# Optimization experiments

Measured on AMD Instinct MI355X. Metric: run time of the kernel, lower is better.

The kernel has to match this reference:

```python
import jax, jax.numpy as jnp
import numpy as np

B, S, D, H = 4, 1024, 1024, 16
HD = D // H
NEG = 10000.0


def setup_inputs() -> dict:
    key = jax.random.key(0)
    k1, k2, k3 = jax.random.split(key, 3)
    std = 0.02
    return {
        "x": jax.random.normal(k1, (B, S, D), dtype=jnp.float32),
        "mask": jnp.zeros((B, 1, 1, S), dtype=jnp.float32),
        "w_attn": jax.random.normal(k2, (D, 3 * D), dtype=jnp.float32) * std,
        "b_attn": jnp.zeros((1, 3 * D), dtype=jnp.float32),
        "w_proj": jax.random.normal(k3, (D, D), dtype=jnp.float32) * std,
        "b_proj": jnp.zeros((1, D), dtype=jnp.float32),
    }


def reference(x, mask, w_attn, b_attn, w_proj, b_proj):
    b, s, d = x.shape
    # fused QKV projection (Conv1D == dense over last dim)
    qkv = x @ w_attn + b_attn  # [B,S,3D]
    q, k, v = jnp.split(qkv, 3, axis=2)

    def split_heads(t):  # [B,S,D] -> [B,H,S,HD]
        return t.reshape(b, s, H, HD).transpose(0, 2, 1, 3)

    q, k, v = split_heads(q), split_heads(k), split_heads(v)

    w = jnp.einsum("bhqd,bhkd->bhqk", q, k) / jnp.sqrt(jnp.float32(HD))
    # causal mask (lower triangle from lower-right corner)
    i = jnp.arange(s)[:, None]
    j = jnp.arange(s)[None, :]
    bmask = (i >= j).astype(w.dtype)[None, None]  # [1,1,S,S]
    w = w * bmask - NEG * (1.0 - bmask)
    w = w + mask
    w = jax.nn.softmax(w, axis=-1)  # attn_dropout is identity at inference
    a = jnp.einsum("bhqk,bhkd->bhqd", w, v)
    a = a.transpose(0, 2, 1, 3).reshape(b, s, d)  # merge heads
    a = a @ w_proj + b_proj  # resid_dropout identity at inference
    return (a, w)
```

## Files before the change

### kernel.cpp

```cpp
#include <hip/hip_runtime.h>
#include <hip/hip_bf16.h>

constexpr int Bb = 4, Ss = 1024, Dd = 1024, Hh = 16;

typedef __attribute__((ext_vector_type(8))) short short8;
typedef __attribute__((ext_vector_type(4))) float f32x4;

static __device__ __forceinline__ ushort f2bf(float f) {
  union { __hip_bfloat16 h; ushort u; } cv;
  cv.h = __float2bfloat16(f);
  return cv.u;
}

static __device__ __forceinline__ void gl_lds16(const ushort* g, ushort* l) {
  __builtin_amdgcn_global_load_lds(
      (const __attribute__((address_space(1))) void*)g,
      (__attribute__((address_space(3))) void*)l, 16, 0, 0);
}

__global__ __launch_bounds__(256) void cast_f32_bf16(
    const float* __restrict__ in, ushort* __restrict__ out) {
  const int i = (blockIdx.x * 256 + threadIdx.x) * 4;
  const float4 v = *(const float4*)&in[i];
  ushort4 o;
  o.x = f2bf(v.x); o.y = f2bf(v.y); o.z = f2bf(v.z); o.w = f2bf(v.w);
  *(ushort4*)&out[i] = o;
}

__global__ __launch_bounds__(256) void transpose_cast(
    const float* __restrict__ in, ushort* __restrict__ out, int R, int C) {
  __shared__ float T[32][33];
  const int c0 = blockIdx.x * 32, r0 = blockIdx.y * 32;
  const int t = threadIdx.x;
  const int r = t >> 3, c4 = (t & 7) * 4;
  const float4 v = *(const float4*)&in[(size_t)(r0 + r) * C + c0 + c4];
  T[r][c4 + 0] = v.x; T[r][c4 + 1] = v.y;
  T[r][c4 + 2] = v.z; T[r][c4 + 3] = v.w;
  __syncthreads();
  const int cc = t >> 3, rr4 = (t & 7) * 4;
  ushort4 o;
  o.x = f2bf(T[rr4 + 0][cc]); o.y = f2bf(T[rr4 + 1][cc]);
  o.z = f2bf(T[rr4 + 2][cc]); o.w = f2bf(T[rr4 + 3][cc]);
  *(ushort4*)&out[(size_t)(c0 + cc) * R + r0 + rr4] = o;
}

template <int BM, int BN, bool OUT_BF16>
__global__ __launch_bounds__(256) void gemm_bt(
    const ushort* __restrict__ A, const ushort* __restrict__ Bt,
    const float* __restrict__ bias, void* __restrict__ Cout,
    int M, int N, int K) {
  constexpr int TM = BM / 32, TN = BN / 32;
  __shared__ ushort As[BM * 32];
  __shared__ ushort Bs[BN * 32];
  const int tid = threadIdx.x;
  const int wv = tid >> 6, lane = tid & 63;
  const int l15 = lane & 15, quad = lane >> 4;
  const int ln4 = lane >> 2, kp = (lane & 3) * 8;
  const int m0 = blockIdx.y * BM, n0 = blockIdx.x * BN;
  const int wrow = (wv >> 1) * (BM / 2), wcol = (wv & 1) * (BN / 2);

  const ushort* Arow = &A[(size_t)(m0 + wv * 16 + ln4) * K + kp];
  const ushort* Brow = &Bt[(size_t)(n0 + wv * 16 + ln4) * K + kp];
  ushort* As_base = &As[wv * 512];
  ushort* Bs_base = &Bs[wv * 512];

  f32x4 acc[TM][TN] = {};

  for (int k0 = 0; k0 < K; k0 += 32) {
#pragma unroll
    for (int u = 0; u < BM / 64; u++)
      gl_lds16(Arow + (size_t)u * 64 * K + k0, As_base + u * 2048);
#pragma unroll
    for (int u = 0; u < BN / 64; u++)
      gl_lds16(Brow + (size_t)u * 64 * K + k0, Bs_base + u * 2048);
    __syncthreads();
    short8 af[TM], bfr[TN];
#pragma unroll
    for (int i = 0; i < TM; i++)
      af[i] = *(const short8*)&As[(wrow + i * 16 + l15) * 32 + quad * 8];
#pragma unroll
    for (int j = 0; j < TN; j++)
      bfr[j] = *(const short8*)&Bs[(wcol + j * 16 + l15) * 32 + quad * 8];
#pragma unroll
    for (int i = 0; i < TM; i++)
#pragma unroll
      for (int j = 0; j < TN; j++)
        acc[i][j] = __builtin_amdgcn_mfma_f32_16x16x32_bf16(af[i], bfr[j],
                                                            acc[i][j], 0, 0, 0);
    __syncthreads();
  }

#pragma unroll
  for (int j = 0; j < TN; j++) {
    const int col = n0 + wcol + j * 16 + l15;
    const float bv = bias[col];
#pragma unroll
    for (int i = 0; i < TM; i++) {
#pragma unroll
      for (int r = 0; r < 4; r++) {
        const int row = m0 + wrow + i * 16 + quad * 4 + r;
        const float v = acc[i][j][r] + bv;
        if (OUT_BF16)
          ((ushort*)Cout)[(size_t)row * N + col] = f2bf(v);
        else
          ((float*)Cout)[(size_t)row * N + col] = v;
      }
    }
  }
}

__global__ __launch_bounds__(256) void vtrans(const ushort* __restrict__ qkvb,
                                              ushort* __restrict__ vt) {
  __shared__ ushort T[64 * 72];
  const int j0 = blockIdx.x * 64, bh = blockIdx.y;
  const int b = bh >> 4, h = bh & 15;
  const int t = threadIdx.x;
#pragma unroll
  for (int u = 0; u < 2; u++) {
    const int idx = t + 256 * u;
    const int row = idx >> 3, p = idx & 7;
    *(uint4*)&T[row * 72 + p * 8] = *(const uint4*)&qkvb[
        (size_t)((b << 10) + j0 + row) * 3072 + 2048 + h * 64 + p * 8];
  }
  __syncthreads();
#pragma unroll
  for (int u = 0; u < 2; u++) {
    const int idx = t + 256 * u;
    const int d = idx >> 3, p = idx & 7;
    ushort tmp[8];
#pragma unroll
    for (int kk = 0; kk < 8; kk++) tmp[kk] = T[(p * 8 + kk) * 72 + d];
    uint4 o;
    __builtin_memcpy(&o, tmp, 16);
    *(uint4*)&vt[((size_t)bh * 64 + d) * 1024 + j0 + p * 8] = o;
  }
}

__global__ __launch_bounds__(256) void attn_mfma(
    const ushort* __restrict__ qkvb,
    const ushort* __restrict__ vt,
    const float* __restrict__ mask,
    float* __restrict__ w_out,
    ushort* __restrict__ ab) {
  constexpr int LDP = 1032;
  __shared__ ushort Ps[16 * LDP];
  __shared__ float PM[16][4];
  __shared__ float PSum[16][4];

  const int f = blockIdx.y * 64 + blockIdx.x;
  const int swz = (f & 7) * 512 + (f >> 3);
  const int qt = swz & 63, bh = swz >> 6;

  const int b = bh >> 4, h = bh & 15;
  const int q0 = qt * 16;
  const int tid = threadIdx.x;
  const int wv = tid >> 6, lane = tid & 63;
  const int l15 = lane & 15, quad = lane >> 4;

  const size_t rowQ = (size_t)((b << 10) + q0 + l15) * 3072 + h * 64;
  const short8 qf0 = *(const short8*)&qkvb[rowQ + quad * 8];
  const short8 qf1 = *(const short8*)&qkvb[rowQ + 32 + quad * 8];

  float sreg[16][4];

#pragma unroll
  for (int i = 0; i < 16; i++) {
    const int j0 = (wv + 4 * i) * 16;
    const int col = j0 + l15;
    const float mv = mask[(b << 10) + col];
    if (j0 <= q0 + 15) {
      const size_t rowK = (size_t)((b << 10) + j0 + l15) * 3072 + 1024 + h * 64;
      const short8 kf0 = *(const short8*)&qkvb[rowK + quad * 8];
      const short8 kf1 = *(const short8*)&qkvb[rowK + 32 + quad * 8];
      f32x4 c = {0.f, 0.f, 0.f, 0.f};
      c = __builtin_amdgcn_mfma_f32_16x16x32_bf16(qf0, kf0, c, 0, 0, 0);
      c = __builtin_amdgcn_mfma_f32_16x16x32_bf16(qf1, kf1, c, 0, 0, 0);
#pragma unroll
      for (int r = 0; r < 4; r++)
        sreg[i][r] =
            (col <= q0 + quad * 4 + r ? c[r] * 0.125f : -10000.0f) + mv;
    } else {
#pragma unroll
      for (int r = 0; r < 4; r++) sreg[i][r] = -10000.0f + mv;
    }
  }

#pragma unroll
  for (int r = 0; r < 4; r++) {
    float m = sreg[0][r];
#pragma unroll
    for (int i = 1; i < 16; i++) m = fmaxf(m, sreg[i][r]);
#pragma unroll
    for (int off = 1; off < 16; off <<= 1) m = fmaxf(m, __shfl_xor(m, off));
    if (l15 == 0) PM[quad * 4 + r][wv] = m;
  }
  __syncthreads();

  float mrow[4];
#pragma unroll
  for (int r = 0; r < 4; r++) {
    const f32x4 pm4 = *(const f32x4*)&PM[quad * 4 + r][0];
    mrow[r] = fmaxf(fmaxf(pm4[0], pm4[1]), fmaxf(pm4[2], pm4[3]));
  }

  float psum[4] = {0.f, 0.f, 0.f, 0.f};
#pragma unroll
  for (int i = 0; i < 16; i++)
#pragma unroll
    for (int r = 0; r < 4; r++) {
      const float e = __expf(fminf(sreg[i][r] - mrow[r], 0.0f));
      sreg[i][r] = e;
      psum[r] += e;
    }
#pragma unroll
  for (int r = 0; r < 4; r++) {
    float s = psum[r];
#pragma unroll
    for (int off = 1; off < 16; off <<= 1) s += __shfl_xor(s, off);
    if (l15 == 0) PSum[quad * 4 + r][wv] = s;
  }
  __syncthreads();

  float inv4[4];
#pragma unroll
  for (int r = 0; r < 4; r++) {
    const f32x4 ps4 = *(const f32x4*)&PSum[quad * 4 + r][0];
    inv4[r] = 1.0f / fmaxf(ps4[0] + ps4[1] + ps4[2] + ps4[3], 1e-30f);
  }

#pragma unroll
  for (int i = 0; i < 16; i++) {
    const int j0 = (wv + 4 * i) * 16;
#pragma unroll
    for (int r = 0; r < 4; r++) {
      const float p = sreg[i][r] * inv4[r];
      w_out[((size_t)(bh << 10) + q0 + quad * 4 + r) * 1024 + j0 + l15] = p;
      Ps[(quad * 4 + r) * LDP + j0 + l15] = f2bf(p);
    }
  }
  __syncthreads();

  f32x4 oacc = {0.f, 0.f, 0.f, 0.f};
  const int nch = (q0 + 16 + 31) >> 5;
  const ushort* vbase = vt + ((size_t)bh * 64 + wv * 16 + l15) * 1024;
  for (int c = 0; c < nch; c++) {
    const int k0 = c * 32;
    const short8 pf = *(const short8*)&Ps[l15 * LDP + k0 + quad * 8];
    const short8 vf = *(const short8*)&vbase[k0 + quad * 8];
    oacc = __builtin_amdgcn_mfma_f32_16x16x32_bf16(pf, vf, oacc, 0, 0, 0);
  }
#pragma unroll
  for (int r = 0; r < 4; r++) {
    ab[(size_t)((b << 10) + q0 + quad * 4 + r) * 1024 + h * 64 + wv * 16 +
       l15] = f2bf(oacc[r]);
  }
}

extern "C" void kernel_launch(void* const* d_in, const int* in_sizes, int n_in,
                              void* d_out, int out_size, void* d_ws,
                              size_t ws_size, hipStream_t stream) {
  const float* x = (const float*)d_in[0];
  const float* mask = (const float*)d_in[1];
  const float* w_attn = (const float*)d_in[2];
  const float* b_attn = (const float*)d_in[3];
  const float* w_proj = (const float*)d_in[4];
  const float* b_proj = (const float*)d_in[5];

  float* out_a = (float*)d_out;
  float* out_w = out_a + (size_t)Bb * Ss * Dd;

  char* ws = (char*)d_ws;
  ushort* xb   = (ushort*)(ws);
  ushort* wta  = (ushort*)(ws + (8u << 20));
  ushort* wtp  = (ushort*)(ws + (14u << 20));
  ushort* qkvb = (ushort*)(ws + (16u << 20));
  ushort* vt   = (ushort*)(ws + (40u << 20));
  ushort* ab   = (ushort*)(ws + (48u << 20));

  cast_f32_bf16<<<(Bb * Ss * Dd) / 1024, 256, 0, stream>>>(x, xb);
  transpose_cast<<<dim3(3 * Dd / 32, Dd / 32), 256, 0, stream>>>(w_attn, wta,
                                                                 Dd, 3 * Dd);
  transpose_cast<<<dim3(Dd / 32, Dd / 32), 256, 0, stream>>>(w_proj, wtp, Dd,
                                                             Dd);
  gemm_bt<128, 128, true><<<dim3(3 * Dd / 128, Bb * Ss / 128), 256, 0,
                            stream>>>(xb, wta, b_attn, qkvb, Bb * Ss, 3 * Dd,
                                      Dd);
  vtrans<<<dim3(Ss / 64, Bb * Hh), 256, 0, stream>>>(qkvb, vt);
  attn_mfma<<<dim3(Ss / 16, Bb * Hh), 256, 0, stream>>>(qkvb, vt, mask, out_w,
                                                        ab);
  gemm_bt<128, 64, false><<<dim3(Dd / 64, Bb * Ss / 128), 256, 0, stream>>>(
      ab, wtp, b_proj, out_a, Bb * Ss, Dd, Dd);
}
```

Before: 448.4 us.

## Double-buffer GEMM LDS tiles and write transposed V directly from QKV GEMM

The GEMM K-loop now uses two LDS buffers, so the next tile's global-to-LDS loads are issued before the MFMAs on the current tile and one of the two barriers per iteration is dropped. The QKV GEMM epilogue writes the V columns straight into the transposed vt layout, which removes the separate vtrans kernel launch and its extra pass over V. The cost is twice the LDS per block, which may lower occupancy, and an extra epilogue branch.

```diff
diff --git a/kernel.cpp b/kernel.cpp
--- a/kernel.cpp
+++ b/kernel.cpp
@@ -44,14 +44,14 @@
   *(ushort4*)&out[(size_t)(c0 + cc) * R + r0 + rr4] = o;
 }
 
-template <int BM, int BN, bool OUT_BF16>
+template <int BM, int BN, bool OUT_BF16, bool V_SPLIT>
 __global__ __launch_bounds__(256) void gemm_bt(
     const ushort* __restrict__ A, const ushort* __restrict__ Bt,
     const float* __restrict__ bias, void* __restrict__ Cout,
-    int M, int N, int K) {
+    ushort* __restrict__ vt, int M, int N, int K) {
   constexpr int TM = BM / 32, TN = BN / 32;
-  __shared__ ushort As[BM * 32];
-  __shared__ ushort Bs[BN * 32];
+  __shared__ ushort As[2][BM * 32];
+  __shared__ ushort Bs[2][BN * 32];
   const int tid = threadIdx.x;
   const int wv = tid >> 6, lane = tid & 63;
   const int l15 = lane & 15, quad = lane >> 4;
@@ -61,26 +61,38 @@
 
   const ushort* Arow = &A[(size_t)(m0 + wv * 16 + ln4) * K + kp];
   const ushort* Brow = &Bt[(size_t)(n0 + wv * 16 + ln4) * K + kp];
-  ushort* As_base = &As[wv * 512];
-  ushort* Bs_base = &Bs[wv * 512];
 
   f32x4 acc[TM][TN] = {};
 
-  for (int k0 = 0; k0 < K; k0 += 32) {
-#pragma unroll
-    for (int u = 0; u < BM / 64; u++)
-      gl_lds16(Arow + (size_t)u * 64 * K + k0, As_base + u * 2048);
-#pragma unroll
-    for (int u = 0; u < BN / 64; u++)
-      gl_lds16(Brow + (size_t)u * 64 * K + k0, Bs_base + u * 2048);
-    __syncthreads();
+#pragma unroll
+  for (int u = 0; u < BM / 64; u++)
+    gl_lds16(Arow + (size_t)u * 64 * K, &As[0][wv * 512 + u * 2048]);
+#pragma unroll
+  for (int u = 0; u < BN / 64; u++)
+    gl_lds16(Brow + (size_t)u * 64 * K, &Bs[0][wv * 512 + u * 2048]);
+  __syncthreads();
+
+  const int nt = K / 32;
+  int cur = 0;
+  for (int t = 0; t < nt; ++t) {
+    if (t + 1 < nt) {
+      const int k1 = (t + 1) * 32;
+#pragma unroll
+      for (int u = 0; u < BM / 64; u++)
+        gl_lds16(Arow + (size_t)u * 64 * K + k1,
+                 &As[cur ^ 1][wv * 512 + u * 2048]);
+#pragma unroll
+      for (int u = 0; u < BN / 64; u++)
+        gl_lds16(Brow + (size_t)u * 64 * K + k1,
+                 &Bs[cur ^ 1][wv * 512 + u * 2048]);
+    }
     short8 af[TM], bfr[TN];
 #pragma unroll
     for (int i = 0; i < TM; i++)
-      af[i] = *(const short8*)&As[(wrow + i * 16 + l15) * 32 + quad * 8];
+      af[i] = *(const short8*)&As[cur][(wrow + i * 16 + l15) * 32 + quad * 8];
 #pragma unroll
     for (int j = 0; j < TN; j++)
-      bfr[j] = *(const short8*)&Bs[(wcol + j * 16 + l15) * 32 + quad * 8];
+      bfr[j] = *(const short8*)&Bs[cur][(wcol + j * 16 + l15) * 32 + quad * 8];
 #pragma unroll
     for (int i = 0; i < TM; i++)
 #pragma unroll
@@ -88,51 +100,46 @@
         acc[i][j] = __builtin_amdgcn_mfma_f32_16x16x32_bf16(af[i], bfr[j],
                                                             acc[i][j], 0, 0, 0);
     __syncthreads();
-  }
-
-#pragma unroll
-  for (int j = 0; j < TN; j++) {
-    const int col = n0 + wcol + j * 16 + l15;
-    const float bv = bias[col];
-#pragma unroll
-    for (int i = 0; i < TM; i++) {
-#pragma unroll
-      for (int r = 0; r < 4; r++) {
-        const int row = m0 + wrow + i * 16 + quad * 4 + r;
-        const float v = acc[i][j][r] + bv;
-        if (OUT_BF16)
-          ((ushort*)Cout)[(size_t)row * N + col] = f2bf(v);
-        else
-          ((float*)Cout)[(size_t)row * N + col] = v;
+    cur ^= 1;
+  }
+
+  if (V_SPLIT && n0 >= 2048) {
+#pragma unroll
+    for (int j = 0; j < TN; j++) {
+      const int col = n0 + wcol + j * 16 + l15;
+      const int cv = col - 2048;
+      const int hh = cv >> 6, dd = cv & 63;
+      const float bv = bias[col];
+#pragma unroll
+      for (int i = 0; i < TM; i++) {
+        const int row0 = m0 + wrow + i * 16 + quad * 4;
+        const int bidx = row0 >> 10, jt = row0 & 1023;
+        ushort4 o;
+        o.x = f2bf(acc[i][j][0] + bv);
+        o.y = f2bf(acc[i][j][1] + bv);
+        o.z = f2bf(acc[i][j][2] + bv);
+        o.w = f2bf(acc[i][j][3] + bv);
+        *(ushort4*)&vt[((size_t)((bidx << 4) + hh) * 64 + dd) * 1024 + jt] = o;
       }
     }
-  }
-}
-
-__global__ __launch_bounds__(256) void vtrans(const ushort* __restrict__ qkvb,
-                                              ushort* __restrict__ vt) {
-  __shared__ ushort T[64 * 72];
-  const int j0 = blockIdx.x * 64, bh = blockIdx.y;
-  const int b = bh >> 4, h = bh & 15;
-  const int t = threadIdx.x;
-#pragma unroll
-  for (int u = 0; u < 2; u++) {
-    const int idx = t + 256 * u;
-    const int row = idx >> 3, p = idx & 7;
-    *(uint4*)&T[row * 72 + p * 8] = *(const uint4*)&qkvb[
-        (size_t)((b << 10) + j0 + row) * 3072 + 2048 + h * 64 + p * 8];
-  }
-  __syncthreads();
-#pragma unroll
-  for (int u = 0; u < 2; u++) {
-    const int idx = t + 256 * u;
-    const int d = idx >> 3, p = idx & 7;
-    ushort tmp[8];
-#pragma unroll
-    for (int kk = 0; kk < 8; kk++) tmp[kk] = T[(p * 8 + kk) * 72 + d];
-    uint4 o;
-    __builtin_memcpy(&o, tmp, 16);
-    *(uint4*)&vt[((size_t)bh * 64 + d) * 1024 + j0 + p * 8] = o;
+  } else {
+#pragma unroll
+    for (int j = 0; j < TN; j++) {
+      const int col = n0 + wcol + j * 16 + l15;
+      const float bv = bias[col];
+#pragma unroll
+      for (int i = 0; i < TM; i++) {
+#pragma unroll
+        for (int r = 0; r < 4; r++) {
+          const int row = m0 + wrow + i * 16 + quad * 4 + r;
+          const float v = acc[i][j][r] + bv;
+          if (OUT_BF16)
+            ((ushort*)Cout)[(size_t)row * N + col] = f2bf(v);
+          else
+            ((float*)Cout)[(size_t)row * N + col] = v;
+        }
+      }
+    }
   }
 }
 
@@ -282,12 +289,12 @@
                                                                  Dd, 3 * Dd);
   transpose_cast<<<dim3(Dd / 32, Dd / 32), 256, 0, stream>>>(w_proj, wtp, Dd,
                                                              Dd);
-  gemm_bt<128, 128, true><<<dim3(3 * Dd / 128, Bb * Ss / 128), 256, 0,
-                            stream>>>(xb, wta, b_attn, qkvb, Bb * Ss, 3 * Dd,
-                                      Dd);
-  vtrans<<<dim3(Ss / 64, Bb * Hh), 256, 0, stream>>>(qkvb, vt);
+  gemm_bt<128, 128, true, true><<<dim3(3 * Dd / 128, Bb * Ss / 128), 256, 0,
+                                  stream>>>(xb, wta, b_attn, qkvb, vt,
+                                            Bb * Ss, 3 * Dd, Dd);
   attn_mfma<<<dim3(Ss / 16, Bb * Hh), 256, 0, stream>>>(qkvb, vt, mask, out_w,
                                                         ab);
-  gemm_bt<128, 64, false><<<dim3(Dd / 64, Bb * Ss / 128), 256, 0, stream>>>(
-      ab, wtp, b_proj, out_a, Bb * Ss, Dd, Dd);
-}
+  gemm_bt<128, 64, false, false><<<dim3(Dd / 64, Bb * Ss / 128), 256, 0,
+                                   stream>>>(ab, wtp, b_proj, out_a, nullptr,
+                                             Bb * Ss, Dd, Dd);
+}
```

Measured after the change: 443.7 us. Within noise of the previous version (-1.0%).
